# Kernel optimization log

Hardware: AMD Instinct MI355X
Metric: run time of the kernel (lower is better)

The kernel has to match this reference:

```python
import jax, jax.numpy as jnp
import numpy as np

EMBED_DIM = 1024
NUM_HEADS = 16
HEAD_DIM = EMBED_DIM // NUM_HEADS
BATCH = 2
SEQ = 2048


def setup_inputs() -> dict:
    key = jax.random.key(0)
    ks = jax.random.split(key, 9)
    s = EMBED_DIM ** -0.5
    inp = {"x": jax.random.normal(ks[0], (BATCH, SEQ, EMBED_DIM), dtype=jnp.float32)}
    names = ["Wq", "Wk", "Wv", "Wo"]
    for i, n in enumerate(names):
        inp[n] = jax.random.normal(ks[1 + i], (EMBED_DIM, EMBED_DIM), dtype=jnp.float32) * s
        inp["b" + n[1]] = jax.random.normal(ks[5 + i], (EMBED_DIM,), dtype=jnp.float32) * 0.02
    return inp


def reference(x, Wq, bq, Wk, bk, Wv, bv, Wo, bo):
    B, S, E = x.shape
    H, D = NUM_HEADS, HEAD_DIM
    scaling = D ** -0.5
    # projections (torch Linear: x @ W.T + b), reshape to (B, H, S, D)
    q = (x @ Wq.T + bq).reshape(B, S, H, D).transpose(0, 2, 1, 3)
    k = (x @ Wk.T + bk).reshape(B, S, H, D).transpose(0, 2, 1, 3)
    v = (x @ Wv.T + bv).reshape(B, S, H, D).transpose(0, 2, 1, 3)
    # full materialized score matrix, matching the original module
    scores = jnp.einsum("bhqd,bhkd->bhqk", q, k) * scaling
    causal = jnp.triu(jnp.ones((S, S), dtype=bool), k=1)  # True above diagonal
    scores = jnp.where(causal[None, None], -jnp.inf, scores)
    attn = jax.nn.softmax(scores, axis=-1)
    out = jnp.einsum("bhqk,bhkd->bhqd", attn, v)  # (B, H, S, D)
    out = out.transpose(0, 2, 1, 3).reshape(B, S, E)
    return out @ Wo.T + bo
```

## Files before the change

kernel.cpp:

```cpp
#include <hip/hip_runtime.h>
#include <stdint.h>

typedef __bf16 bf16;
typedef __bf16 bf16x8 __attribute__((ext_vector_type(8)));
typedef __bf16 bf16x4 __attribute__((ext_vector_type(4)));
typedef float  f32x4  __attribute__((ext_vector_type(4)));

#define E_DIM 1024
#define S_LEN 2048
#define BATCH 2
#define NH 16
#define DH 64

#define NEG_INF (-__builtin_inff())

__device__ __forceinline__ void load_lds16(const bf16* g, bf16* l) {
    __builtin_amdgcn_global_load_lds(
        (const __attribute__((address_space(1))) void*)g,
        (__attribute__((address_space(3))) void*)l, 16, 0, 0);
}

__global__ __launch_bounds__(256) void convert_kernel(
    const float* __restrict__ s0, const float* __restrict__ s1,
    const float* __restrict__ s2, const float* __restrict__ s3,
    const float* __restrict__ s4,
    bf16* __restrict__ d0, bf16* __restrict__ d1, bf16* __restrict__ d2,
    bf16* __restrict__ d3, bf16* __restrict__ d4,
    int n0, int n1)
{
    const float* src; bf16* dst; int n;
    switch (blockIdx.y) {
        case 0:  src = s0; dst = d0; n = n0; break;
        case 1:  src = s1; dst = d1; n = n1; break;
        case 2:  src = s2; dst = d2; n = n1; break;
        case 3:  src = s3; dst = d3; n = n1; break;
        default: src = s4; dst = d4; n = n1; break;
    }
    int i = (blockIdx.x * 256 + threadIdx.x) * 4;
    if (i >= n) return;
    float4 v = *(const float4*)(src + i);
    bf16x4 o;
    o[0] = (bf16)v.x; o[1] = (bf16)v.y; o[2] = (bf16)v.z; o[3] = (bf16)v.w;
    *(bf16x4*)(dst + i) = o;
}

__global__ __launch_bounds__(256) void gemm_kernel(
    const bf16* __restrict__ A,
    const bf16* __restrict__ W0, const bf16* __restrict__ W1, const bf16* __restrict__ W2,
    const float* __restrict__ bias0, const float* __restrict__ bias1, const float* __restrict__ bias2,
    bf16* __restrict__ outQ, bf16* __restrict__ outK, bf16* __restrict__ outVt,
    float* __restrict__ outF, int final_mode)
{
    __shared__ bf16 As[2][128 * 32];
    __shared__ bf16 Bs[2][128 * 32];

    int mode;
    const bf16* W; const float* bias;
    if (final_mode) { mode = 3; W = W0; bias = bias0; }
    else {
        mode = blockIdx.z;
        W    = (mode == 0) ? W0 : (mode == 1 ? W1 : W2);
        bias = (mode == 0) ? bias0 : (mode == 1 ? bias1 : bias2);
    }

    const int bm = blockIdx.y * 128, bn = blockIdx.x * 128;
    const int t = threadIdx.x;
    const int lane = t & 63, w = t >> 6;
    const int quad = lane >> 4, l16 = lane & 15;
    const int wm = (w & 1) * 64, wn = (w >> 1) * 64;

    const int r0 = w * 16;
    const int srow = r0 + (lane >> 2), scol = (lane & 3) * 8;
    const bf16* Ag0 = A + (size_t)(bm + srow) * E_DIM + scol;
    const bf16* Ag1 = Ag0 + (size_t)64 * E_DIM;
    const bf16* Wg0 = W + (size_t)(bn + srow) * E_DIM + scol;
    const bf16* Wg1 = Wg0 + (size_t)64 * E_DIM;

    f32x4 acc[4][4];
#pragma unroll
    for (int i = 0; i < 4; i++)
#pragma unroll
        for (int j = 0; j < 4; j++) acc[i][j] = f32x4{0.f, 0.f, 0.f, 0.f};

    load_lds16(Ag0, As[0] + r0 * 32);
    load_lds16(Ag1, As[0] + (64 + r0) * 32);
    load_lds16(Wg0, Bs[0] + r0 * 32);
    load_lds16(Wg1, Bs[0] + (64 + r0) * 32);

    int cur = 0;
    for (int kt = 0; kt < E_DIM; kt += 32) {
        __syncthreads();

        if (kt + 32 < E_DIM) {
            const int nxt = cur ^ 1;
            load_lds16(Ag0 + kt + 32, As[nxt] + r0 * 32);
            load_lds16(Ag1 + kt + 32, As[nxt] + (64 + r0) * 32);
            load_lds16(Wg0 + kt + 32, Bs[nxt] + r0 * 32);
            load_lds16(Wg1 + kt + 32, Bs[nxt] + (64 + r0) * 32);
        }

        bf16x8 af[4], bfr[4];
#pragma unroll
        for (int i = 0; i < 4; i++)
            af[i] = *(const bf16x8*)(As[cur] + (wm + i * 16 + l16) * 32 + quad * 8);
#pragma unroll
        for (int j = 0; j < 4; j++)
            bfr[j] = *(const bf16x8*)(Bs[cur] + (wn + j * 16 + l16) * 32 + quad * 8);
#pragma unroll
        for (int i = 0; i < 4; i++)
#pragma unroll
            for (int j = 0; j < 4; j++)
                acc[i][j] = __builtin_amdgcn_mfma_f32_16x16x32_bf16(af[i], bfr[j], acc[i][j], 0, 0, 0);

        cur ^= 1;
    }

#pragma unroll
    for (int j = 0; j < 4; j++) {
        const int n = bn + wn + j * 16 + l16;
        const float bv = bias[n];
#pragma unroll
        for (int i = 0; i < 4; i++) {
            const int m0 = bm + wm + i * 16 + quad * 4;
            if (mode == 3) {
#pragma unroll
                for (int r = 0; r < 4; r++)
                    outF[(size_t)(m0 + r) * E_DIM + n] = acc[i][j][r] + bv;
            } else if (mode == 2) {
                const int b_ = m0 >> 11, s0 = m0 & (S_LEN - 1);
                const int h = n >> 6, d = n & 63;
                bf16x4 pv;
#pragma unroll
                for (int r = 0; r < 4; r++) pv[r] = (bf16)(acc[i][j][r] + bv);
                *(bf16x4*)(outVt + ((size_t)((b_ * NH + h) * DH + d)) * S_LEN + s0) = pv;
            } else {
                bf16* o = (mode == 0) ? outQ : outK;
                const float sc = (mode == 0) ? 0.125f : 1.0f;
                const int h = n >> 6, d = n & 63;
#pragma unroll
                for (int r = 0; r < 4; r++) {
                    const int m = m0 + r;
                    const int b_ = m >> 11, s = m & (S_LEN - 1);
                    o[((size_t)(b_ * NH + h) * S_LEN + s) * DH + d] = (bf16)((acc[i][j][r] + bv) * sc);
                }
            }
        }
    }
}

__global__ __launch_bounds__(512, 2) void attn_kernel(
    const bf16* __restrict__ Qb, const bf16* __restrict__ Kb,
    const bf16* __restrict__ Vtb, bf16* __restrict__ Ob)
{
    __shared__ bf16 Ks[128 * 72];
    __shared__ bf16 Vs[64 * 136];
    __shared__ bf16 Ps[8][16 * 136];

    const int t = threadIdx.x, lane = t & 63, w = t >> 6;
    const int quad = lane >> 4, l16 = lane & 15;

    const int i = blockIdx.x;
    const int xcd = i & 7, rr = i >> 3;
    const int bh = (xcd << 2) | (rr & 3);
    const int pr = rr >> 2;
    const int qlo = pr, qhi = 15 - pr;

    const bf16* Qg = Qb + (size_t)bh * S_LEN * DH;
    const bf16* Kg = Kb + (size_t)bh * S_LEN * DH;
    const bf16* Vg = Vtb + (size_t)bh * DH * S_LEN;
    const int b_ = bh >> 4, h = bh & 15;
    bf16* Og = Ob + (size_t)b_ * S_LEN * E_DIM + h * DH;

    bf16* Pw = Ps[w];
    const int inrow0 = w * 16;

    bf16x8 aq[2][2];
#pragma unroll
    for (int qt = 0; qt < 2; qt++) {
        const int qrow0 = (qt ? qhi : qlo) * 128 + inrow0;
        const bf16* qp = Qg + (size_t)(qrow0 + l16) * DH + quad * 8;
        aq[qt][0] = *(const bf16x8*)(qp);
        aq[qt][1] = *(const bf16x8*)(qp + 32);
    }

    f32x4 o[2][4];
    float l_part[2][4];
#pragma unroll
    for (int qt = 0; qt < 2; qt++)
#pragma unroll
        for (int dt = 0; dt < 4; dt++) {
            o[qt][dt] = f32x4{0.f, 0.f, 0.f, 0.f};
            l_part[qt][dt] = 0.f;
        }

    const int T = qhi + 1;
    const int kr0 = t >> 3, kce = (t & 7) * 8;
    const int vr0 = t >> 4, vce = (t & 15) * 8;

    for (int kt = 0; kt < T; kt++) {
        const int kb = kt * 128;
        uint4 k0 = *(const uint4*)(Kg + (size_t)(kb + kr0) * DH + kce);
        uint4 k1 = *(const uint4*)(Kg + (size_t)(kb + kr0 + 64) * DH + kce);
        uint4 v0 = *(const uint4*)(Vg + (size_t)vr0 * S_LEN + kb + vce);
        uint4 v1 = *(const uint4*)(Vg + (size_t)(vr0 + 32) * S_LEN + kb + vce);
        __syncthreads();
        *(uint4*)(Ks + kr0 * 72 + kce) = k0;
        *(uint4*)(Ks + (kr0 + 64) * 72 + kce) = k1;
        *(uint4*)(Vs + vr0 * 136 + vce) = v0;
        *(uint4*)(Vs + (vr0 + 32) * 136 + vce) = v1;
        __syncthreads();

#pragma unroll
        for (int qt = 0; qt < 2; qt++) {
            if (qt == 0 && kt > qlo) continue;
            const bool diag = qt ? (kt == qhi) : (kt == qlo);
            const int irb = inrow0 + quad * 4;

#pragma unroll
            for (int jt = 0; jt < 8; jt++) {
                const bf16* kp = Ks + (jt * 16 + l16) * 72 + quad * 8;
                bf16x8 bk0 = *(const bf16x8*)(kp);
                bf16x8 bk1 = *(const bf16x8*)(kp + 32);
                f32x4 s = f32x4{0.f, 0.f, 0.f, 0.f};
                s = __builtin_amdgcn_mfma_f32_16x16x32_bf16(aq[qt][0], bk0, s, 0, 0, 0);
                s = __builtin_amdgcn_mfma_f32_16x16x32_bf16(aq[qt][1], bk1, s, 0, 0, 0);
                const int kcol = jt * 16 + l16;
#pragma unroll
                for (int r = 0; r < 4; r++) {
                    float sval = s[r];
                    if (diag && kcol > irb + r) sval = NEG_INF;
                    const float pe = __expf(sval);
                    l_part[qt][r] += pe;
                    Pw[(quad * 4 + r) * 136 + jt * 16 + l16] = (bf16)pe;
                }
            }

#pragma unroll
            for (int ks = 0; ks < 4; ks++) {
                bf16x8 ap = *(const bf16x8*)(Pw + l16 * 136 + ks * 32 + quad * 8);
#pragma unroll
                for (int dt = 0; dt < 4; dt++) {
                    bf16x8 bv = *(const bf16x8*)(Vs + (dt * 16 + l16) * 136 + ks * 32 + quad * 8);
                    o[qt][dt] = __builtin_amdgcn_mfma_f32_16x16x32_bf16(ap, bv, o[qt][dt], 0, 0, 0);
                }
            }
        }
    }

#pragma unroll
    for (int qt = 0; qt < 2; qt++) {
        const int qrow0 = (qt ? qhi : qlo) * 128 + inrow0;
#pragma unroll
        for (int r = 0; r < 4; r++) {
            float l = l_part[qt][r];
            l += __shfl_xor(l, 1);
            l += __shfl_xor(l, 2);
            l += __shfl_xor(l, 4);
            l += __shfl_xor(l, 8);
            l_part[qt][r] = 1.0f / l;
        }
#pragma unroll
        for (int r = 0; r < 4; r++) {
            const int srow = qrow0 + quad * 4 + r;
#pragma unroll
            for (int dt = 0; dt < 4; dt++)
                Og[(size_t)srow * E_DIM + dt * 16 + l16] =
                    (bf16)(o[qt][dt][r] * l_part[qt][r]);
        }
    }
}

extern "C" void kernel_launch(void* const* d_in, const int* in_sizes, int n_in,
                              void* d_out, int out_size, void* d_ws, size_t ws_size,
                              hipStream_t stream)
{
    const float* x  = (const float*)d_in[0];
    const float* Wq = (const float*)d_in[1];
    const float* bq = (const float*)d_in[2];
    const float* Wk = (const float*)d_in[3];
    const float* bk = (const float*)d_in[4];
    const float* Wv = (const float*)d_in[5];
    const float* bv = (const float*)d_in[6];
    const float* Wo = (const float*)d_in[7];
    const float* bo = (const float*)d_in[8];
    float* out = (float*)d_out;

    char* ws = (char*)d_ws;
    const size_t MB = 1ull << 20;
    bf16* xb  = (bf16*)(ws + 0);
    bf16* wqb = (bf16*)(ws + 8 * MB);
    bf16* wkb = (bf16*)(ws + 10 * MB);
    bf16* wvb = (bf16*)(ws + 12 * MB);
    bf16* wob = (bf16*)(ws + 14 * MB);
    bf16* Qb  = (bf16*)(ws + 16 * MB);
    bf16* Kb  = (bf16*)(ws + 24 * MB);
    bf16* Vtb = (bf16*)(ws + 32 * MB);
    bf16* Ab  = (bf16*)(ws + 40 * MB);

    convert_kernel<<<dim3(4096, 5), 256, 0, stream>>>(
        x, Wq, Wk, Wv, Wo, xb, wqb, wkb, wvb, wob, 4194304, 1048576);

    gemm_kernel<<<dim3(8, 32, 3), 256, 0, stream>>>(
        xb, wqb, wkb, wvb, bq, bk, bv, Qb, Kb, Vtb, nullptr, 0);

    attn_kernel<<<dim3(256), 512, 0, stream>>>(Qb, Kb, Vtb, Ab);

    gemm_kernel<<<dim3(8, 32, 1), 256, 0, stream>>>(
        Ab, wob, wob, wob, bo, bo, bo, nullptr, nullptr, nullptr, out, 1);
}
```

Baseline: 199.4 us.

## Restructure attention to keep P in registers and split keys across warps

Rewrites the attention kernel so each block handles one query tile, with 512 blocks instead of 256 paired tiles. Warps split the 128-key tile into two halves. Scores are computed transposed (K·Q) so the probabilities can be packed to bf16 and rearranged with permlane swaps, removing the P round-trip through LDS. K/V loads for the next tile are prefetched into registers, exp uses exp2 with log2e folded into the Q scale, and the two key-half partials are reduced through LDS at the end. Occupancy hint is raised to 4 blocks; the design relies on no running max, as before, and adds a final cross-warp reduction.

Result: faster. 193.3 us (-3.1%).

```diff
diff --git a/kernel.cpp b/kernel.cpp
--- a/kernel.cpp
+++ b/kernel.cpp
@@ -5,6 +5,7 @@
 typedef __bf16 bf16x8 __attribute__((ext_vector_type(8)));
 typedef __bf16 bf16x4 __attribute__((ext_vector_type(4)));
 typedef float  f32x4  __attribute__((ext_vector_type(4)));
+typedef unsigned int u32;
 
 #define E_DIM 1024
 #define S_LEN 2048
@@ -13,6 +14,20 @@
 #define DH 64
 
 #define NEG_INF (-__builtin_inff())
+
+union BU { u32 u[4]; bf16x8 h; };
+
+__device__ __forceinline__ u32 cvtpk_bf16(float lo, float hi) {
+    u32 r;
+    asm("v_cvt_pk_bf16_f32 %0, %1, %2" : "=v"(r) : "v"(lo), "v"(hi));
+    return r;
+}
+__device__ __forceinline__ void pswap32(u32 &a, u32 &b) {
+    asm("v_permlane32_swap_b32 %0, %1" : "+v"(a), "+v"(b));
+}
+__device__ __forceinline__ void pswap16(u32 &a, u32 &b) {
+    asm("v_permlane16_swap_b32 %0, %1" : "+v"(a), "+v"(b));
+}
 
 __device__ __forceinline__ void load_lds16(const bf16* g, bf16* l) {
     __builtin_amdgcn_global_load_lds(
@@ -135,7 +150,7 @@
                 *(bf16x4*)(outVt + ((size_t)((b_ * NH + h) * DH + d)) * S_LEN + s0) = pv;
             } else {
                 bf16* o = (mode == 0) ? outQ : outK;
-                const float sc = (mode == 0) ? 0.125f : 1.0f;
+                const float sc = (mode == 0) ? 0.18033688f : 1.0f;
                 const int h = n >> 6, d = n & 63;
 #pragma unroll
                 for (int r = 0; r < 4; r++) {
@@ -148,61 +163,60 @@
     }
 }
 
-__global__ __launch_bounds__(512, 2) void attn_kernel(
+__global__ __launch_bounds__(512, 4) void attn_kernel(
     const bf16* __restrict__ Qb, const bf16* __restrict__ Kb,
     const bf16* __restrict__ Vtb, bf16* __restrict__ Ob)
 {
-    __shared__ bf16 Ks[128 * 72];
-    __shared__ bf16 Vs[64 * 136];
-    __shared__ bf16 Ps[8][16 * 136];
+    __shared__ __align__(16) char smem[35840];
+    bf16* Ks = (bf16*)smem;
+    bf16* Vs = (bf16*)(smem + 18432);
 
     const int t = threadIdx.x, lane = t & 63, w = t >> 6;
     const int quad = lane >> 4, l16 = lane & 15;
+    const int qs = w & 3, kh = w >> 2;
 
     const int i = blockIdx.x;
-    const int xcd = i & 7, rr = i >> 3;
+    const int half = i >> 8, jj = i & 255;
+    const int xcd = jj & 7, rr = jj >> 3;
     const int bh = (xcd << 2) | (rr & 3);
-    const int pr = rr >> 2;
-    const int qlo = pr, qhi = 15 - pr;
+    const int qq = rr >> 2;
+    const int qt = half ? qq : 15 - qq;
 
     const bf16* Qg = Qb + (size_t)bh * S_LEN * DH;
     const bf16* Kg = Kb + (size_t)bh * S_LEN * DH;
     const bf16* Vg = Vtb + (size_t)bh * DH * S_LEN;
-    const int b_ = bh >> 4, h = bh & 15;
-    bf16* Og = Ob + (size_t)b_ * S_LEN * E_DIM + h * DH;
-
-    bf16* Pw = Ps[w];
-    const int inrow0 = w * 16;
-
-    bf16x8 aq[2][2];
-#pragma unroll
-    for (int qt = 0; qt < 2; qt++) {
-        const int qrow0 = (qt ? qhi : qlo) * 128 + inrow0;
-        const bf16* qp = Qg + (size_t)(qrow0 + l16) * DH + quad * 8;
-        aq[qt][0] = *(const bf16x8*)(qp);
-        aq[qt][1] = *(const bf16x8*)(qp + 32);
+    const int b_ = bh >> 4, hh = bh & 15;
+    bf16* Og = Ob + (size_t)b_ * S_LEN * E_DIM + hh * DH;
+
+    const int qrow0 = qt * 128 + qs * 32;
+
+    bf16x8 qf[2][2];
+#pragma unroll
+    for (int qh = 0; qh < 2; qh++) {
+        const bf16* qp = Qg + (size_t)(qrow0 + qh * 16 + l16) * DH + quad * 8;
+        qf[qh][0] = *(const bf16x8*)(qp);
+        qf[qh][1] = *(const bf16x8*)(qp + 32);
     }
 
     f32x4 o[2][4];
-    float l_part[2][4];
-#pragma unroll
-    for (int qt = 0; qt < 2; qt++)
-#pragma unroll
-        for (int dt = 0; dt < 4; dt++) {
-            o[qt][dt] = f32x4{0.f, 0.f, 0.f, 0.f};
-            l_part[qt][dt] = 0.f;
-        }
-
-    const int T = qhi + 1;
+    f32x4 lacc[2];
+#pragma unroll
+    for (int qh = 0; qh < 2; qh++) {
+        lacc[qh] = f32x4{0.f, 0.f, 0.f, 0.f};
+#pragma unroll
+        for (int dt = 0; dt < 4; dt++) o[qh][dt] = f32x4{0.f, 0.f, 0.f, 0.f};
+    }
+
+    const int T = qt + 1;
     const int kr0 = t >> 3, kce = (t & 7) * 8;
     const int vr0 = t >> 4, vce = (t & 15) * 8;
 
+    uint4 k0 = *(const uint4*)(Kg + (size_t)kr0 * DH + kce);
+    uint4 k1 = *(const uint4*)(Kg + (size_t)(kr0 + 64) * DH + kce);
+    uint4 v0 = *(const uint4*)(Vg + (size_t)vr0 * S_LEN + vce);
+    uint4 v1 = *(const uint4*)(Vg + (size_t)(vr0 + 32) * S_LEN + vce);
+
     for (int kt = 0; kt < T; kt++) {
-        const int kb = kt * 128;
-        uint4 k0 = *(const uint4*)(Kg + (size_t)(kb + kr0) * DH + kce);
-        uint4 k1 = *(const uint4*)(Kg + (size_t)(kb + kr0 + 64) * DH + kce);
-        uint4 v0 = *(const uint4*)(Vg + (size_t)vr0 * S_LEN + kb + vce);
-        uint4 v1 = *(const uint4*)(Vg + (size_t)(vr0 + 32) * S_LEN + kb + vce);
         __syncthreads();
         *(uint4*)(Ks + kr0 * 72 + kce) = k0;
         *(uint4*)(Ks + (kr0 + 64) * 72 + kce) = k1;
@@ -210,62 +224,112 @@
         *(uint4*)(Vs + (vr0 + 32) * 136 + vce) = v1;
         __syncthreads();
 
-#pragma unroll
-        for (int qt = 0; qt < 2; qt++) {
-            if (qt == 0 && kt > qlo) continue;
-            const bool diag = qt ? (kt == qhi) : (kt == qlo);
-            const int irb = inrow0 + quad * 4;
-
-#pragma unroll
-            for (int jt = 0; jt < 8; jt++) {
-                const bf16* kp = Ks + (jt * 16 + l16) * 72 + quad * 8;
-                bf16x8 bk0 = *(const bf16x8*)(kp);
-                bf16x8 bk1 = *(const bf16x8*)(kp + 32);
-                f32x4 s = f32x4{0.f, 0.f, 0.f, 0.f};
-                s = __builtin_amdgcn_mfma_f32_16x16x32_bf16(aq[qt][0], bk0, s, 0, 0, 0);
-                s = __builtin_amdgcn_mfma_f32_16x16x32_bf16(aq[qt][1], bk1, s, 0, 0, 0);
-                const int kcol = jt * 16 + l16;
-#pragma unroll
-                for (int r = 0; r < 4; r++) {
-                    float sval = s[r];
-                    if (diag && kcol > irb + r) sval = NEG_INF;
-                    const float pe = __expf(sval);
-                    l_part[qt][r] += pe;
-                    Pw[(quad * 4 + r) * 136 + jt * 16 + l16] = (bf16)pe;
+        if (kt + 1 < T) {
+            const int kb = (kt + 1) * 128;
+            k0 = *(const uint4*)(Kg + (size_t)(kb + kr0) * DH + kce);
+            k1 = *(const uint4*)(Kg + (size_t)(kb + kr0 + 64) * DH + kce);
+            v0 = *(const uint4*)(Vg + (size_t)vr0 * S_LEN + kb + vce);
+            v1 = *(const uint4*)(Vg + (size_t)(vr0 + 32) * S_LEN + kb + vce);
+        }
+
+        const bool diag = (kt == qt);
+
+#pragma unroll
+        for (int itp = 0; itp < 2; itp++) {
+            f32x4 p[2][2];
+#pragma unroll
+            for (int e = 0; e < 2; e++) {
+                const int itg = kh * 4 + itp * 2 + e;
+                const bf16* kp = Ks + (itg * 16 + l16) * 72 + quad * 8;
+                bf16x8 kf0 = *(const bf16x8*)(kp);
+                bf16x8 kf1 = *(const bf16x8*)(kp + 32);
+#pragma unroll
+                for (int qh = 0; qh < 2; qh++) {
+                    f32x4 s = __builtin_amdgcn_mfma_f32_16x16x32_bf16(
+                        kf0, qf[qh][0], f32x4{0.f, 0.f, 0.f, 0.f}, 0, 0, 0);
+                    s = __builtin_amdgcn_mfma_f32_16x16x32_bf16(
+                        kf1, qf[qh][1], s, 0, 0, 0);
+                    if (diag) {
+                        const int kloc = kh * 64 + (itp * 2 + e) * 16 + quad * 4;
+                        const int qloc = qs * 32 + qh * 16 + l16;
+#pragma unroll
+                        for (int r = 0; r < 4; r++)
+                            if (kloc + r > qloc) s[r] = NEG_INF;
+                    }
+                    f32x4 pe;
+#pragma unroll
+                    for (int r = 0; r < 4; r++) pe[r] = exp2f(s[r]);
+                    lacc[qh] += pe;
+                    p[qh][e] = pe;
                 }
             }
 
-#pragma unroll
-            for (int ks = 0; ks < 4; ks++) {
-                bf16x8 ap = *(const bf16x8*)(Pw + l16 * 136 + ks * 32 + quad * 8);
-#pragma unroll
-                for (int dt = 0; dt < 4; dt++) {
-                    bf16x8 bv = *(const bf16x8*)(Vs + (dt * 16 + l16) * 136 + ks * 32 + quad * 8);
-                    o[qt][dt] = __builtin_amdgcn_mfma_f32_16x16x32_bf16(ap, bv, o[qt][dt], 0, 0, 0);
-                }
-            }
-        }
-    }
-
-#pragma unroll
-    for (int qt = 0; qt < 2; qt++) {
-        const int qrow0 = (qt ? qhi : qlo) * 128 + inrow0;
-#pragma unroll
-        for (int r = 0; r < 4; r++) {
-            float l = l_part[qt][r];
-            l += __shfl_xor(l, 1);
-            l += __shfl_xor(l, 2);
-            l += __shfl_xor(l, 4);
-            l += __shfl_xor(l, 8);
-            l_part[qt][r] = 1.0f / l;
-        }
-#pragma unroll
-        for (int r = 0; r < 4; r++) {
-            const int srow = qrow0 + quad * 4 + r;
+            BU bu0, bu1;
+            {
+                u32 a0 = cvtpk_bf16(p[0][0][0], p[0][0][1]);
+                u32 a1 = cvtpk_bf16(p[0][0][2], p[0][0][3]);
+                u32 b0 = cvtpk_bf16(p[0][1][0], p[0][1][1]);
+                u32 b1 = cvtpk_bf16(p[0][1][2], p[0][1][3]);
+                pswap32(a0, b0); pswap16(a0, b0);
+                pswap32(a1, b1); pswap16(a1, b1);
+                bu0.u[0] = a0; bu0.u[1] = a1; bu0.u[2] = b0; bu0.u[3] = b1;
+            }
+            {
+                u32 a0 = cvtpk_bf16(p[1][0][0], p[1][0][1]);
+                u32 a1 = cvtpk_bf16(p[1][0][2], p[1][0][3]);
+                u32 b0 = cvtpk_bf16(p[1][1][0], p[1][1][1]);
+                u32 b1 = cvtpk_bf16(p[1][1][2], p[1][1][3]);
+                pswap32(a0, b0); pswap16(a0, b0);
+                pswap32(a1, b1); pswap16(a1, b1);
+                bu1.u[0] = a0; bu1.u[1] = a1; bu1.u[2] = b0; bu1.u[3] = b1;
+            }
+
+            const int ksg = kh * 2 + itp;
+#pragma unroll
+            for (int dt = 0; dt < 4; dt++) {
+                bf16x8 vf = *(const bf16x8*)(Vs + (dt * 16 + l16) * 136 + ksg * 32 + quad * 8);
+                o[0][dt] = __builtin_amdgcn_mfma_f32_16x16x32_bf16(vf, bu0.h, o[0][dt], 0, 0, 0);
+                o[1][dt] = __builtin_amdgcn_mfma_f32_16x16x32_bf16(vf, bu1.h, o[1][dt], 0, 0, 0);
+            }
+        }
+    }
+
+    float lsum[2];
+#pragma unroll
+    for (int qh = 0; qh < 2; qh++) {
+        float l = lacc[qh][0] + lacc[qh][1] + lacc[qh][2] + lacc[qh][3];
+        l += __shfl_xor(l, 16);
+        l += __shfl_xor(l, 32);
+        lsum[qh] = l;
+    }
+
+    __syncthreads();
+    f32x4* Or = (f32x4*)smem;
+    float*  Lr = (float*)(smem + 32768);
+
+    if (kh == 1) {
+#pragma unroll
+        for (int qh = 0; qh < 2; qh++) {
 #pragma unroll
             for (int dt = 0; dt < 4; dt++)
-                Og[(size_t)srow * E_DIM + dt * 16 + l16] =
-                    (bf16)(o[qt][dt][r] * l_part[qt][r]);
+                Or[(((qs * 2 + qh) * 4 + dt) * 4 + quad) * 16 + l16] = o[qh][dt];
+            if (quad == 0) Lr[(qs * 2 + qh) * 16 + l16] = lsum[qh];
+        }
+    }
+    __syncthreads();
+    if (kh == 0) {
+#pragma unroll
+        for (int qh = 0; qh < 2; qh++) {
+            const float inv = 1.0f / (lsum[qh] + Lr[(qs * 2 + qh) * 16 + l16]);
+            const int qg = qrow0 + qh * 16 + l16;
+#pragma unroll
+            for (int dt = 0; dt < 4; dt++) {
+                f32x4 ov = o[qh][dt] + Or[(((qs * 2 + qh) * 4 + dt) * 4 + quad) * 16 + l16];
+                bf16x4 w4;
+#pragma unroll
+                for (int r = 0; r < 4; r++) w4[r] = (bf16)(ov[r] * inv);
+                *(bf16x4*)(Og + (size_t)qg * E_DIM + dt * 16 + quad * 4) = w4;
+            }
         }
     }
 }
@@ -303,7 +367,7 @@
     gemm_kernel<<<dim3(8, 32, 3), 256, 0, stream>>>(
         xb, wqb, wkb, wvb, bq, bk, bv, Qb, Kb, Vtb, nullptr, 0);
 
-    attn_kernel<<<dim3(256), 512, 0, stream>>>(Qb, Kb, Vtb, Ab);
+    attn_kernel<<<dim3(512), 512, 0, stream>>>(Qb, Kb, Vtb, Ab);
 
     gemm_kernel<<<dim3(8, 32, 1), 256, 0, stream>>>(
         Ab, wob, wob, wob, bo, bo, bo, nullptr, nullptr, nullptr, out, 1);
```
